# Kernel optimization log

Hardware: AMD Instinct MI355X
Metric: run time of the kernel (lower is better)

## Reference

```python
import jax, jax.numpy as jnp
import numpy as np

NUM_WIRES = 20
BATCH = 32
DIM = 2 ** NUM_WIRES


def setup_inputs() -> dict:
    key = jax.random.key(0)
    k1, k2, k3 = jax.random.split(key, 3)
    state = jax.random.normal(k1, (BATCH, DIM), dtype=jnp.float32)
    state = state / jnp.linalg.norm(state, axis=1, keepdims=True)  # valid quantum states
    params = jax.random.normal(k2, (2 * NUM_WIRES,), dtype=jnp.float32)
    W = jax.random.normal(k3, (1, NUM_WIRES), dtype=jnp.float32) * 0.1
    b = jnp.zeros((1,), dtype=jnp.float32)
    return {"state": state, "params": params, "W": W, "b": b}


def _apply_1q(psi, U, wire):
    # psi: [B, 2^n] complex; apply 2x2 unitary U on `wire` (wire 0 = most significant axis,
    # matching PennyLane's big-endian wire ordering).
    B = psi.shape[0]
    left = 2 ** wire
    psi4 = psi.reshape(B, left, 2, -1)
    psi4 = jnp.einsum('ts,bisj->bitj', U, psi4)
    return psi4.reshape(B, DIM)


def _apply_cnot(psi, ctrl):
    # CNOT on adjacent wires (ctrl, ctrl+1): swap target amplitudes where control=1.
    B = psi.shape[0]
    left = 2 ** ctrl
    psi5 = psi.reshape(B, left, 2, 2, -1)
    top = psi5[:, :, 0]
    bot = psi5[:, :, 1, ::-1]
    return jnp.stack([top, bot], axis=2).reshape(B, DIM)


def _circuit(state, params):
    psi = state.astype(jnp.complex64)
    for i in range(NUM_WIRES):
        # RX(theta_i)
        c = jnp.cos(params[i] / 2).astype(jnp.complex64)
        s = jnp.sin(params[i] / 2)
        RX = jnp.stack([jnp.stack([c, -1j * s]), jnp.stack([-1j * s, c])])
        psi = _apply_1q(psi, RX, i)
        # RY(theta_{i+n})
        c2 = jnp.cos(params[i + NUM_WIRES] / 2).astype(jnp.complex64)
        s2 = jnp.sin(params[i + NUM_WIRES] / 2).astype(jnp.complex64)
        RY = jnp.stack([jnp.stack([c2, -s2]), jnp.stack([s2, c2])])
        psi = _apply_1q(psi, RY, i)
    for i in range(NUM_WIRES - 1):
        psi = _apply_cnot(psi, i)
    # <Z_i> = sum over basis states of |amp|^2 * (+1 if bit_i==0 else -1)
    probs = psi.real ** 2 + psi.imag ** 2  # [B, 2^n] float32
    B = probs.shape[0]
    feats = []
    for i in range(NUM_WIRES):
        p = probs.reshape(B, 2 ** i, 2, -1)
        feats.append(p[:, :, 0].sum(axis=(1, 2)) - p[:, :, 1].sum(axis=(1, 2)))
    return jnp.stack(feats, axis=1)  # [B, n]


def reference(state, params, W, b):
    feats = _circuit(state, params)          # [B, num_wires]
    out = feats @ W.T + b                    # Linear head
    return out.squeeze(-1)                   # [B]
```

## Files before the change

### kernel.cpp

```cpp
#include <hip/hip_runtime.h>
#include <hip/hip_fp16.h>

#define NW 20

typedef _Float16 h2 __attribute__((ext_vector_type(2)));

struct PkW7 { h2 a, d, dn, e, en, f, fn, pad; };

__device__ __forceinline__ h2 pkrtz(float lo, float hi) {
    typedef __fp16 f16x2 __attribute__((ext_vector_type(2)));
    f16x2 v = __builtin_amdgcn_cvt_pkrtz(lo, hi);
    return *reinterpret_cast<h2*>(&v);
}
__device__ __forceinline__ unsigned h2u(h2 v) { return *reinterpret_cast<unsigned*>(&v); }
__device__ __forceinline__ h2 u2h(unsigned v) { return *reinterpret_cast<h2*>(&v); }

template<int JB>
__device__ __forceinline__ void stage16s(h2 (&xr)[16], h2 (&xi)[16], const PkW7 u) {
    #pragma unroll
    for (int base = 0; base < 16; ++base)
        if (!(base & (1 << JB))) {
            const int p = base | (1 << JB);
            h2 x0r = xr[base], x0i = xi[base], x1r = xr[p], x1i = xi[p];
            xr[base] = u.a * x0r + u.dn * x0i + u.en * x1r + u.f  * x1i;
            xi[base] = u.a * x0i + u.d  * x0r + u.en * x1i + u.fn * x1r;
            xr[p]    = u.e * x0r + u.f  * x0i + u.a  * x1r + u.d  * x1i;
            xi[p]    = u.e * x0i + u.fn * x0r + u.a  * x1i + u.dn * x1r;
        }
}

__global__ void setupk(const float* __restrict__ params, float* __restrict__ cbuf) {
    int w = threadIdx.x;
    if (w < NW) {
        double s1, c1, s2, c2;
        sincos(0.5 * (double)params[w],      &s1, &c1);
        sincos(0.5 * (double)params[w + NW], &s2, &c2);
        float a = (float)(c1 * c2), d = (float)(s1 * s2);
        float e = (float)(s2 * c1), f = (float)(c2 * s1);
        if (w == 19) {
            cbuf[0] = a * 1024.f; cbuf[1] = d * 1024.f;
            cbuf[2] = e * 1024.f; cbuf[3] = f * 1024.f;
        }
        PkW7 pw;
        pw.a.x  = (_Float16) a; pw.a.y  = (_Float16) a;
        pw.d.x  = (_Float16) d; pw.d.y  = (_Float16) d;
        pw.dn.x = (_Float16)-d; pw.dn.y = (_Float16)-d;
        pw.e.x  = (_Float16) e; pw.e.y  = (_Float16) e;
        pw.en.x = (_Float16)-e; pw.en.y = (_Float16)-e;
        pw.f.x  = (_Float16) f; pw.f.y  = (_Float16) f;
        pw.fn.x = (_Float16)-f; pw.fn.y = (_Float16)-f;
        pw.pad.x = (_Float16)0.f; pw.pad.y = (_Float16)0.f;
        ((PkW7*)(cbuf + 4))[w] = pw;
    }
}

__global__ __launch_bounds__(256, 8) void pass1(const float* __restrict__ state,
                                                const float* __restrict__ cbuf,
                                                uint2* __restrict__ amp) {
    __shared__ h2 L[4224];
    const int t     = threadIdx.x;
    const int pr    = blockIdx.x >> 8;
    const int chunk = blockIdx.x & 255;
    const PkW7* PW = (const PkW7*)(cbuf + 4);
    const float a19 = cbuf[0], d19 = cbuf[1], e19 = cbuf[2], f19 = cbuf[3];

    const float4* s0 = (const float4*)(state + ((size_t)pr << 20) + ((size_t)chunk << 12));
    const float4* s1 = (const float4*)((const float*)s0 + ((size_t)16 << 20));

    h2 xr[16], xi[16];
    #pragma unroll
    for (int k = 0; k < 4; ++k) {
        float4 v0 = s0[k * 256 + t];
        float4 v1 = s1[k * 256 + t];
        float r0a = fmaf(a19, v0.x, -e19 * v0.y), i0a = fmaf( d19, v0.x, -f19 * v0.y);
        float r1a = fmaf(e19, v0.x,  a19 * v0.y), i1a = fmaf(-f19, v0.x, -d19 * v0.y);
        float r0b = fmaf(a19, v1.x, -e19 * v1.y), i0b = fmaf( d19, v1.x, -f19 * v1.y);
        float r1b = fmaf(e19, v1.x,  a19 * v1.y), i1b = fmaf(-f19, v1.x, -d19 * v1.y);
        xr[4*k+0] = pkrtz(r0a, r0b); xi[4*k+0] = pkrtz(i0a, i0b);
        xr[4*k+1] = pkrtz(r1a, r1b); xi[4*k+1] = pkrtz(i1a, i1b);
        r0a = fmaf(a19, v0.z, -e19 * v0.w); i0a = fmaf( d19, v0.z, -f19 * v0.w);
        r1a = fmaf(e19, v0.z,  a19 * v0.w); i1a = fmaf(-f19, v0.z, -d19 * v0.w);
        r0b = fmaf(a19, v1.z, -e19 * v1.w); i0b = fmaf( d19, v1.z, -f19 * v1.w);
        r1b = fmaf(e19, v1.z,  a19 * v1.w); i1b = fmaf(-f19, v1.z, -d19 * v1.w);
        xr[4*k+2] = pkrtz(r0a, r0b); xi[4*k+2] = pkrtz(i0a, i0b);
        xr[4*k+3] = pkrtz(r1a, r1b); xi[4*k+3] = pkrtz(i1a, i1b);
    }
    stage16s<1>(xr, xi, PW[18]);
    stage16s<2>(xr, xi, PW[9]);
    stage16s<3>(xr, xi, PW[8]);

    const int p1 = 4 * t + (t >> 3);
    const int p2 = (t & 3) + 66 * (t >> 2);
    #pragma unroll
    for (int r = 0; r < 16; ++r) L[p1 + (r & 3) + 1056 * (r >> 2)] = xr[r];
    __syncthreads();
    #pragma unroll
    for (int r = 0; r < 16; ++r) { const int c = 4 * (r & 3) + 16 * (r >> 2); xr[r] = L[p2 + c + (c >> 5)]; }
    __syncthreads();
    #pragma unroll
    for (int r = 0; r < 16; ++r) L[p1 + (r & 3) + 1056 * (r >> 2)] = xi[r];
    __syncthreads();
    #pragma unroll
    for (int r = 0; r < 16; ++r) { const int c = 4 * (r & 3) + 16 * (r >> 2); xi[r] = L[p2 + c + (c >> 5)]; }

    stage16s<0>(xr, xi, PW[17]);
    stage16s<1>(xr, xi, PW[16]);
    stage16s<2>(xr, xi, PW[15]);
    stage16s<3>(xr, xi, PW[14]);

    const int p3 = (t & 63) + ((t & 63) >> 5) + 1056 * (t >> 6);
    #pragma unroll
    for (int r = 0; r < 16; ++r) { const int c = 4 * (r & 3) + 16 * (r >> 2); L[p2 + c + (c >> 5)] = xr[r]; }
    __syncthreads();
    #pragma unroll
    for (int r = 0; r < 16; ++r) xr[r] = L[p3 + 66 * (r & 3) + 264 * (r >> 2)];
    __syncthreads();
    #pragma unroll
    for (int r = 0; r < 16; ++r) { const int c = 4 * (r & 3) + 16 * (r >> 2); L[p2 + c + (c >> 5)] = xi[r]; }
    __syncthreads();
    #pragma unroll
    for (int r = 0; r < 16; ++r) xi[r] = L[p3 + 66 * (r & 3) + 264 * (r >> 2)];

    stage16s<0>(xr, xi, PW[13]);
    stage16s<1>(xr, xi, PW[12]);
    stage16s<2>(xr, xi, PW[11]);
    stage16s<3>(xr, xi, PW[10]);

    uint2* dst = amp + ((size_t)pr << 20) + ((size_t)chunk << 12);
    const int sbase = (t & 63) + 1024 * (t >> 6);
    #pragma unroll
    for (int r = 0; r < 16; ++r) {
        uint2 w; w.x = h2u(xr[r]); w.y = h2u(xi[r]);
        dst[sbase + 64 * (r & 3) + 256 * (r >> 2)] = w;
    }
}

__global__ __launch_bounds__(256, 8) void pass2(const uint2* __restrict__ amp,
                                                const float* __restrict__ cbuf,
                                                const float* __restrict__ Wv,
                                                float* __restrict__ pws) {
    __shared__ h2     L[4224];
    __shared__ float2 Asig[256];
    __shared__ float  Btab[16];
    __shared__ float  wred[8];
    const int t        = threadIdx.x;
    const int pr       = blockIdx.x >> 8;
    const int chunk    = blockIdx.x & 255;
    const int low_base = chunk * 16;
    const int l = t & 15, hi = t >> 4;
    const PkW7* PW = (const PkW7*)(cbuf + 4);

    {
        float A = 0.f;
        #pragma unroll
        for (int i = 0; i < 8; ++i)
            A += Wv[i] * (1.f - 2.f * (float)(__popc(t >> (7 - i)) & 1));
        Asig[t] = make_float2(A, 1.f - 2.f * (float)(__popc(t) & 1));
    }
    if (t < 16) {
        int low = low_base + t;
        float Bs = 0.f;
        #pragma unroll
        for (int i = 8; i < 20; ++i)
            Bs += Wv[i] * (1.f - 2.f * (float)(__popc(low >> (19 - i)) & 1));
        Btab[t] = Bs;
    }

    const uint2* src = amp + ((size_t)pr << 20) + low_base + l;
    h2 xr[16], xi[16];
    #pragma unroll
    for (int r = 0; r < 16; ++r) {
        uint2 w = src[(size_t)(hi * 16 + r) * 4096];
        xr[r] = u2h(w.x); xi[r] = u2h(w.y);
    }
    stage16s<0>(xr, xi, PW[7]);
    stage16s<1>(xr, xi, PW[6]);
    stage16s<2>(xr, xi, PW[5]);
    stage16s<3>(xr, xi, PW[4]);

    const int p = 264 * hi + l;
    const int q = t + (t >> 5);
    #pragma unroll
    for (int r = 0; r < 16; ++r) L[p + 16 * r + (r >> 1)] = xr[r];
    __syncthreads();
    #pragma unroll
    for (int r = 0; r < 16; ++r) xr[r] = L[q + 264 * r];
    __syncthreads();
    #pragma unroll
    for (int r = 0; r < 16; ++r) L[p + 16 * r + (r >> 1)] = xi[r];
    __syncthreads();
    #pragma unroll
    for (int r = 0; r < 16; ++r) xi[r] = L[q + 264 * r];

    stage16s<0>(xr, xi, PW[3]);
    stage16s<1>(xr, xi, PW[2]);
    stage16s<2>(xr, xi, PW[1]);
    stage16s<3>(xr, xi, PW[0]);

    const float Bl = Btab[l];
    float acc0 = 0.f, acc1 = 0.f;
    #pragma unroll
    for (int r = 0; r < 16; ++r) {
        float vrx = (float)xr[r].x, vry = (float)xr[r].y;
        float vix = (float)xi[r].x, viy = (float)xi[r].y;
        float2 as = Asig[r * 16 + hi];
        float g = fmaf(as.y, Bl, as.x);
        acc0 = fmaf(fmaf(vrx, vrx, vix * vix), g, acc0);
        acc1 = fmaf(fmaf(vry, vry, viy * viy), g, acc1);
    }
    #pragma unroll
    for (int off = 32; off > 0; off >>= 1) {
        acc0 += __shfl_down(acc0, off, 64);
        acc1 += __shfl_down(acc1, off, 64);
    }
    if ((t & 63) == 0) { wred[(t >> 6) * 2] = acc0; wred[(t >> 6) * 2 + 1] = acc1; }
    __syncthreads();
    if (t < 2)
        pws[blockIdx.x * 2 + t] = (wred[t] + wred[2 + t]) + (wred[4 + t] + wred[6 + t]);
}

__global__ void finalk(const float* __restrict__ pws, const float* __restrict__ bias,
                       float* __restrict__ out) {
    const int t = threadIdx.x;
    const int b = t >> 3, j = t & 7;
    const int pr = b & 15, sl = b >> 4;
    float s = 0.f;
    #pragma unroll 4
    for (int k = 0; k < 32; ++k) {
        const int c = j * 32 + k;
        s += pws[(pr * 256 + c) * 2 + sl];
    }
    s += __shfl_down(s, 4, 8);
    s += __shfl_down(s, 2, 8);
    s += __shfl_down(s, 1, 8);
    if (j == 0) out[b] = s * (1.f / 1048576.f) + bias[0];
}

extern "C" void kernel_launch(void* const* d_in, const int* in_sizes, int n_in,
                              void* d_out, int out_size, void* d_ws, size_t ws_size,
                              hipStream_t stream) {
    const float* state  = (const float*)d_in[0];
    const float* params = (const float*)d_in[1];
    const float* Wv     = (const float*)d_in[2];
    const float* bias   = (const float*)d_in[3];
    float* out = (float*)d_out;

    const size_t AMPB = (size_t)16 * (1u << 20) * 8;
    uint2* amp  = (uint2*)d_ws;
    float* pws  = (float*)((char*)d_ws + AMPB);
    float* cbuf = (float*)((char*)d_ws + AMPB + 65536);

    setupk<<<1, 64, 0, stream>>>(params, cbuf);
    pass1 <<<16 * 256, 256, 0, stream>>>(state, cbuf, amp);
    pass2 <<<16 * 256, 256, 0, stream>>>(amp, cbuf, Wv, pws);
    finalk<<<1, 256, 0, stream>>>(pws, bias, out);
}
```

Baseline: 106.7 us.

## Process two chunks per pass1 block with software-prefetched state loads

pass1 now handles two consecutive chunks per block, halving the grid, and issues the second chunk's global loads during the first chunk's LDS transposes so memory latency overlaps compute. Loads use nontemporal hints to avoid polluting cache with streamed input. The change adds an extra barrier and keeps eight more float4 vectors live, raising register pressure, and halves the number of blocks available to hide latency.

```diff
diff --git a/kernel.cpp b/kernel.cpp
--- a/kernel.cpp
+++ b/kernel.cpp
@@ -4,6 +4,7 @@
 #define NW 20
 
 typedef _Float16 h2 __attribute__((ext_vector_type(2)));
+typedef float    f4 __attribute__((ext_vector_type(4)));
 
 struct PkW7 { h2 a, d, dn, e, en, f, fn, pad; };
 
@@ -54,24 +55,16 @@
     }
 }
 
-__global__ __launch_bounds__(256, 8) void pass1(const float* __restrict__ state,
-                                                const float* __restrict__ cbuf,
-                                                uint2* __restrict__ amp) {
-    __shared__ h2 L[4224];
-    const int t     = threadIdx.x;
-    const int pr    = blockIdx.x >> 8;
-    const int chunk = blockIdx.x & 255;
-    const PkW7* PW = (const PkW7*)(cbuf + 4);
-    const float a19 = cbuf[0], d19 = cbuf[1], e19 = cbuf[2], f19 = cbuf[3];
-
-    const float4* s0 = (const float4*)(state + ((size_t)pr << 20) + ((size_t)chunk << 12));
-    const float4* s1 = (const float4*)((const float*)s0 + ((size_t)16 << 20));
-
+template<bool PF>
+__device__ __forceinline__ void do_chunk(int t, h2* L, const PkW7* PW,
+                                         float a19, float d19, float e19, float f19,
+                                         f4 (&va)[4], f4 (&vb)[4],
+                                         const f4* ns0, const f4* ns1,
+                                         uint2* dst) {
     h2 xr[16], xi[16];
     #pragma unroll
     for (int k = 0; k < 4; ++k) {
-        float4 v0 = s0[k * 256 + t];
-        float4 v1 = s1[k * 256 + t];
+        f4 v0 = va[k], v1 = vb[k];
         float r0a = fmaf(a19, v0.x, -e19 * v0.y), i0a = fmaf( d19, v0.x, -f19 * v0.y);
         float r1a = fmaf(e19, v0.x,  a19 * v0.y), i1a = fmaf(-f19, v0.x, -d19 * v0.y);
         float r0b = fmaf(a19, v1.x, -e19 * v1.y), i0b = fmaf( d19, v1.x, -f19 * v1.y);
@@ -94,6 +87,13 @@
     #pragma unroll
     for (int r = 0; r < 16; ++r) L[p1 + (r & 3) + 1056 * (r >> 2)] = xr[r];
     __syncthreads();
+    if (PF) {
+        #pragma unroll
+        for (int k = 0; k < 4; ++k) {
+            va[k] = __builtin_nontemporal_load(ns0 + k * 256 + t);
+            vb[k] = __builtin_nontemporal_load(ns1 + k * 256 + t);
+        }
+    }
     #pragma unroll
     for (int r = 0; r < 16; ++r) { const int c = 4 * (r & 3) + 16 * (r >> 2); xr[r] = L[p2 + c + (c >> 5)]; }
     __syncthreads();
@@ -109,6 +109,7 @@
     stage16s<3>(xr, xi, PW[14]);
 
     const int p3 = (t & 63) + ((t & 63) >> 5) + 1056 * (t >> 6);
+    __syncthreads();
     #pragma unroll
     for (int r = 0; r < 16; ++r) { const int c = 4 * (r & 3) + 16 * (r >> 2); L[p2 + c + (c >> 5)] = xr[r]; }
     __syncthreads();
@@ -126,13 +127,43 @@
     stage16s<2>(xr, xi, PW[11]);
     stage16s<3>(xr, xi, PW[10]);
 
-    uint2* dst = amp + ((size_t)pr << 20) + ((size_t)chunk << 12);
     const int sbase = (t & 63) + 1024 * (t >> 6);
     #pragma unroll
     for (int r = 0; r < 16; ++r) {
         uint2 w; w.x = h2u(xr[r]); w.y = h2u(xi[r]);
         dst[sbase + 64 * (r & 3) + 256 * (r >> 2)] = w;
     }
+}
+
+__global__ __launch_bounds__(256, 8) void pass1(const float* __restrict__ state,
+                                                const float* __restrict__ cbuf,
+                                                uint2* __restrict__ amp) {
+    __shared__ h2 L[4224];
+    const int t  = threadIdx.x;
+    const int pr = blockIdx.x >> 7;
+    const int g  = blockIdx.x & 127;
+    const PkW7* PW = (const PkW7*)(cbuf + 4);
+    const float a19 = cbuf[0], d19 = cbuf[1], e19 = cbuf[2], f19 = cbuf[3];
+
+    const float* base0 = state + ((size_t)pr << 20);
+    const float* base1 = base0 + ((size_t)16 << 20);
+    const f4* sA0 = (const f4*)(base0 + ((size_t)(2 * g)     << 12));
+    const f4* sA1 = (const f4*)(base1 + ((size_t)(2 * g)     << 12));
+    const f4* sB0 = (const f4*)(base0 + ((size_t)(2 * g + 1) << 12));
+    const f4* sB1 = (const f4*)(base1 + ((size_t)(2 * g + 1) << 12));
+
+    f4 va[4], vb[4];
+    #pragma unroll
+    for (int k = 0; k < 4; ++k) {
+        va[k] = __builtin_nontemporal_load(sA0 + k * 256 + t);
+        vb[k] = __builtin_nontemporal_load(sA1 + k * 256 + t);
+    }
+
+    uint2* dstA = amp + ((size_t)pr << 20) + ((size_t)(2 * g) << 12);
+    do_chunk<true>(t, L, PW, a19, d19, e19, f19, va, vb, sB0, sB1, dstA);
+
+    __syncthreads();
+    do_chunk<false>(t, L, PW, a19, d19, e19, f19, va, vb, sB0, sB1, dstA + 4096);
 }
 
 __global__ __launch_bounds__(256, 8) void pass2(const uint2* __restrict__ amp,
@@ -251,7 +282,7 @@
     float* cbuf = (float*)((char*)d_ws + AMPB + 65536);
 
     setupk<<<1, 64, 0, stream>>>(params, cbuf);
-    pass1 <<<16 * 256, 256, 0, stream>>>(state, cbuf, amp);
+    pass1 <<<16 * 128, 256, 0, stream>>>(state, cbuf, amp);
     pass2 <<<16 * 256, 256, 0, stream>>>(amp, cbuf, Wv, pws);
     finalk<<<1, 256, 0, stream>>>(pws, bias, out);
 }
```

After: 126.3 us. 1.18x slower.

## Replace one LDS transpose round in pass1 with wavefront shuffle gate stages

Applied to the files above, without the earlier changes.

Six gate stages in pass1 (wires 17..12) now run as cross-lane __shfl_xor butterflies instead of in-register stages that needed a second shared-memory transpose. This removes one full LDS write/read round trip and its barriers for both real and imaginary parts. In exchange, each shuffle stage issues 32 cross-lane shuffles plus extra selects per thread. Correctness depends on the lane-to-index mapping matching the bit positions the removed transpose used to handle.

```diff
diff --git a/kernel.cpp b/kernel.cpp
--- a/kernel.cpp
+++ b/kernel.cpp
@@ -4,6 +4,7 @@
 #define NW 20
 
 typedef _Float16 h2 __attribute__((ext_vector_type(2)));
+typedef float    f4 __attribute__((ext_vector_type(4)));
 
 struct PkW7 { h2 a, d, dn, e, en, f, fn, pad; };
 
@@ -27,6 +28,24 @@
             xr[p]    = u.e * x0r + u.f  * x0i + u.a  * x1r + u.d  * x1i;
             xi[p]    = u.e * x0i + u.fn * x0r + u.a  * x1i + u.dn * x1r;
         }
+}
+
+template<int JB>
+__device__ __forceinline__ void shufstage(h2 (&xr)[16], h2 (&xi)[16], const PkW7 u, int t) {
+    const bool hi_ = (t >> JB) & 1;
+    const h2 ds_  = hi_ ? u.d  : u.dn;
+    const h2 nds_ = hi_ ? u.dn : u.d;
+    const h2 es_  = hi_ ? u.e  : u.en;
+    #pragma unroll
+    for (int r = 0; r < 16; ++r) {
+        h2 or_ = xr[r], oi_ = xi[r];
+        int pri = __shfl_xor(*reinterpret_cast<int*>(&or_), 1 << JB, 64);
+        int pii = __shfl_xor(*reinterpret_cast<int*>(&oi_), 1 << JB, 64);
+        h2 pr_ = *reinterpret_cast<h2*>(&pri);
+        h2 pi_ = *reinterpret_cast<h2*>(&pii);
+        xr[r] = u.a * or_ + ds_  * oi_ + es_ * pr_ + u.f  * pi_;
+        xi[r] = u.a * oi_ + nds_ * or_ + es_ * pi_ + u.fn * pr_;
+    }
 }
 
 __global__ void setupk(const float* __restrict__ params, float* __restrict__ cbuf) {
@@ -64,14 +83,14 @@
     const PkW7* PW = (const PkW7*)(cbuf + 4);
     const float a19 = cbuf[0], d19 = cbuf[1], e19 = cbuf[2], f19 = cbuf[3];
 
-    const float4* s0 = (const float4*)(state + ((size_t)pr << 20) + ((size_t)chunk << 12));
-    const float4* s1 = (const float4*)((const float*)s0 + ((size_t)16 << 20));
+    const f4* s0 = (const f4*)(state + ((size_t)pr << 20) + ((size_t)chunk << 12));
+    const f4* s1 = (const f4*)((const float*)s0 + ((size_t)16 << 20));
 
     h2 xr[16], xi[16];
     #pragma unroll
     for (int k = 0; k < 4; ++k) {
-        float4 v0 = s0[k * 256 + t];
-        float4 v1 = s1[k * 256 + t];
+        f4 v0 = s0[k * 256 + t];
+        f4 v1 = s1[k * 256 + t];
         float r0a = fmaf(a19, v0.x, -e19 * v0.y), i0a = fmaf( d19, v0.x, -f19 * v0.y);
         float r1a = fmaf(e19, v0.x,  a19 * v0.y), i1a = fmaf(-f19, v0.x, -d19 * v0.y);
         float r0b = fmaf(a19, v1.x, -e19 * v1.y), i0b = fmaf( d19, v1.x, -f19 * v1.y);
@@ -89,49 +108,36 @@
     stage16s<2>(xr, xi, PW[9]);
     stage16s<3>(xr, xi, PW[8]);
 
+    shufstage<0>(xr, xi, PW[17], t);
+    shufstage<1>(xr, xi, PW[16], t);
+    shufstage<2>(xr, xi, PW[15], t);
+    shufstage<3>(xr, xi, PW[14], t);
+    shufstage<4>(xr, xi, PW[13], t);
+    shufstage<5>(xr, xi, PW[12], t);
+
     const int p1 = 4 * t + (t >> 3);
-    const int p2 = (t & 3) + 66 * (t >> 2);
+    const int q  = (t & 63) + ((t & 63) >> 5) + 1056 * (t >> 6);
     #pragma unroll
     for (int r = 0; r < 16; ++r) L[p1 + (r & 3) + 1056 * (r >> 2)] = xr[r];
     __syncthreads();
     #pragma unroll
-    for (int r = 0; r < 16; ++r) { const int c = 4 * (r & 3) + 16 * (r >> 2); xr[r] = L[p2 + c + (c >> 5)]; }
+    for (int r = 0; r < 16; ++r) xr[r] = L[q + 66 * (r & 3) + 264 * (r >> 2)];
     __syncthreads();
     #pragma unroll
     for (int r = 0; r < 16; ++r) L[p1 + (r & 3) + 1056 * (r >> 2)] = xi[r];
     __syncthreads();
     #pragma unroll
-    for (int r = 0; r < 16; ++r) { const int c = 4 * (r & 3) + 16 * (r >> 2); xi[r] = L[p2 + c + (c >> 5)]; }
-
-    stage16s<0>(xr, xi, PW[17]);
-    stage16s<1>(xr, xi, PW[16]);
-    stage16s<2>(xr, xi, PW[15]);
-    stage16s<3>(xr, xi, PW[14]);
-
-    const int p3 = (t & 63) + ((t & 63) >> 5) + 1056 * (t >> 6);
-    #pragma unroll
-    for (int r = 0; r < 16; ++r) { const int c = 4 * (r & 3) + 16 * (r >> 2); L[p2 + c + (c >> 5)] = xr[r]; }
-    __syncthreads();
-    #pragma unroll
-    for (int r = 0; r < 16; ++r) xr[r] = L[p3 + 66 * (r & 3) + 264 * (r >> 2)];
-    __syncthreads();
-    #pragma unroll
-    for (int r = 0; r < 16; ++r) { const int c = 4 * (r & 3) + 16 * (r >> 2); L[p2 + c + (c >> 5)] = xi[r]; }
-    __syncthreads();
-    #pragma unroll
-    for (int r = 0; r < 16; ++r) xi[r] = L[p3 + 66 * (r & 3) + 264 * (r >> 2)];
-
-    stage16s<0>(xr, xi, PW[13]);
-    stage16s<1>(xr, xi, PW[12]);
+    for (int r = 0; r < 16; ++r) xi[r] = L[q + 66 * (r & 3) + 264 * (r >> 2)];
+
     stage16s<2>(xr, xi, PW[11]);
     stage16s<3>(xr, xi, PW[10]);
 
     uint2* dst = amp + ((size_t)pr << 20) + ((size_t)chunk << 12);
-    const int sbase = (t & 63) + 1024 * (t >> 6);
+    const int sb = (t & 63) + 1024 * (t >> 6);
     #pragma unroll
     for (int r = 0; r < 16; ++r) {
         uint2 w; w.x = h2u(xr[r]); w.y = h2u(xi[r]);
-        dst[sbase + 64 * (r & 3) + 256 * (r >> 2)] = w;
+        dst[sb + 64 * (r & 3) + 256 * (r >> 2)] = w;
     }
 }
 
```

New measurement: 109.7 us. 1.03x slower.
